# Optimization experiments

Measured on AMD Instinct MI355X. Metric: run time of the kernel, lower is better.

The kernel has to match this reference:

```python
import jax, jax.numpy as jnp
from jax import lax
import numpy as np

P = 16          # patch_len
EPS = 1e-5      # BatchNorm eps


def _dct_mats(L):
    # torch_dct DCT-II: ortho matrix Co and scale d s.t. dct(norm=None)(x) = (x @ Co.T) * d,
    # dct(norm='ortho')(x) = x @ Co.T, idct(norm=None)(y) = (y / d) @ Co
    n = jnp.arange(L, dtype=jnp.float32)
    base = jnp.cos(jnp.pi * (2.0 * n[None, :] + 1.0) * n[:, None] / (2.0 * L))
    ck = jnp.where(n == 0, 1.0 / jnp.sqrt(jnp.float32(L)), jnp.sqrt(2.0 / L))
    Co = base * ck[:, None]
    d = jnp.where(n == 0, 2.0 * jnp.sqrt(jnp.float32(L)), jnp.sqrt(2.0 * L))
    return Co, d


def _gelu(t):
    return jax.nn.gelu(t, approximate=False)  # torch nn.GELU default (erf)


def _dw(t, w, pad):  # depthwise Conv1d, t [B,D,L], w [D,k], SAME-style padding
    return lax.conv_general_dilated(t, w[:, None, :], (1,), [(pad, pad)],
                                    feature_group_count=t.shape[1],
                                    dimension_numbers=('NCH', 'OIH', 'NCH'))


def _forward(x, conv1_w, conv1_b, conv2_w, conv2_b, conv3_w, conv3_b,
             dn_g, dn_b, dn_m, dn_v, pn_g, pn_b, pn_m, pn_v,
             embed_w, embed_b, lin_res_w, lin_res_b,
             depth_res_w, depth_res_b, depth_conv_w, depth_conv_b,
             threshold, att_dw_w, att_dw_b, att_conv_w, att_conv_b,
             att_g, att_b, att_m, att_v, fc1_w, fc1_b, fc2_w, fc2_b):
    B, L, D = x.shape
    N = L // P                       # patch_num (stride == patch_len)
    Co, dvec = _dct_mats(L)

    conv1 = lambda t: t * conv1_w[:, None] + conv1_b[:, None]   # grouped 1x1 Conv1d
    bnD = lambda t: (t - dn_m[:, None]) * (dn_g[:, None] / jnp.sqrt(dn_v[:, None] + EPS)) + dn_b[:, None]

    xt = jnp.transpose(x, (0, 2, 1))                 # [B,D,L]
    freq_res = conv1(xt)
    z_dct = (xt @ Co.T) * dvec                       # dct(norm=None)

    # adaptive high-frequency mask
    energy = jnp.sum(z_dct * z_dct, axis=-1)         # [B,D]
    med = jnp.median(energy, axis=1, keepdims=True)
    ne = energy / (med + 1e-6)
    thr = lax.stop_gradient(jnp.quantile(ne, jnp.clip(threshold[0], 0.0, 1.0)))
    mask = (ne > thr).astype(x.dtype)[..., None]     # rows of dominant vars -> 1
    z = _gelu(conv1(z_dct * mask))
    z1 = (z / dvec) @ Co + freq_res                  # idct(norm=None) + residual

    # patching (stride == patch_len -> unfold is a reshape)
    z_p = xt.reshape(B * D, N, P) @ embed_w + embed_b            # [BD,N,P*P]
    z_res = (z_p.reshape(B, D, -1) @ lin_res_w + lin_res_b).transpose(0, 2, 1)  # [B,pred,D]
    time_res = z_p @ depth_res_w + depth_res_b                   # [BD,N,P]
    # depth_conv: grouped Conv1d kernel=stride=P over d_model=P*P
    z_depth = jnp.einsum('bnpj,nj->bnp', z_p.reshape(B * D, N, P, P), depth_conv_w) \
              + depth_conv_b[None, :, None] + time_res
    z_depth = (z_depth - pn_m[:, None]) * (pn_g[:, None] / jnp.sqrt(pn_v[:, None] + EPS)) + pn_b[:, None]
    z2 = _gelu(z_depth).reshape(B, D, L)

    z2_f = conv1(bnD(_gelu((z2 @ Co.T) * dvec)))

    z_r = jax.nn.sigmoid(conv1(bnD(_gelu(_dw(z1, conv2_w, 2) + conv2_b[:, None]))))
    zg = _gelu(z2_f * z_r)

    z1b = _gelu(bnD(_dw(z1, conv3_w, 3) + conv3_b[:, None]))
    z1c = bnD(zg) + z1b

    # DctAtt on z1c * z2: ortho DCT, take 5 low-freq comps per var
    xa = (z1c * z2) @ Co.T                            # [B,D,L]
    low = xa[:, :, :5].reshape(B, D, 5)               # concat layout matches torch loop
    zd = jnp.einsum('bdj,j->bd', low, att_dw_w) + att_dw_b[0]   # Conv1d(1,1,5,stride=5)
    zd = _gelu(zd)
    zd = (zd - att_m[0]) * (att_g[0] / jnp.sqrt(att_v[0] + EPS)) + att_b[0]  # BN(1)
    zd = zd * att_conv_w[0] + att_conv_b[0]           # Conv1d(1,1,1)
    att1 = jax.nn.softmax(zd, axis=-1)[..., None]     # [B,D,1]

    zf = z1c * att1 + z2 * (1.0 - att1)
    out = _gelu(zf @ fc1_w + fc1_b) @ fc2_w + fc2_b   # Mlp -> [B,D,pred]
    return z_res + out.transpose(0, 2, 1)             # [B,pred,D]


def setup_inputs() -> dict:
    key = jax.random.key(0)
    ks = iter(jax.random.split(key, 48))
    B, L, D, pred = 32, 512, 321, 96
    N, dm = L // P, P * P
    r = lambda shape, s=1.0: jax.random.normal(next(ks), shape, jnp.float32) * s
    return dict(
        x=r((B, L, D)),
        conv1_w=r((D,), 0.5) + 1.0, conv1_b=r((D,), 0.1),
        conv2_w=r((D, 5), 0.3), conv2_b=r((D,), 0.1),
        conv3_w=r((D, 7), 0.3), conv3_b=r((D,), 0.1),
        dn_g=jnp.ones((D,), jnp.float32), dn_b=jnp.zeros((D,), jnp.float32),
        dn_m=r((D,), 0.1), dn_v=jnp.ones((D,), jnp.float32),
        pn_g=jnp.ones((N,), jnp.float32), pn_b=jnp.zeros((N,), jnp.float32),
        pn_m=r((N,), 0.1), pn_v=jnp.ones((N,), jnp.float32),
        embed_w=r((P, dm), 0.25), embed_b=r((dm,), 0.02),
        lin_res_w=r((N * dm, pred), 0.01), lin_res_b=r((pred,), 0.02),
        depth_res_w=r((dm, P), 0.06), depth_res_b=r((P,), 0.02),
        depth_conv_w=r((N, P), 0.25), depth_conv_b=r((N,), 0.02),
        threshold=jax.random.uniform(next(ks), (1,), jnp.float32) * 0.5,
        att_dw_w=r((5,), 0.4), att_dw_b=r((1,), 0.1),
        att_conv_w=r((1,)), att_conv_b=r((1,), 0.1),
        att_g=jnp.ones((1,), jnp.float32), att_b=jnp.zeros((1,), jnp.float32),
        att_m=jnp.zeros((1,), jnp.float32), att_v=jnp.ones((1,), jnp.float32),
        fc1_w=r((L, pred), 0.04), fc1_b=r((pred,), 0.02),
        fc2_w=r((pred, pred), 0.1), fc2_b=r((pred,), 0.02),
    )


def reference(x, conv1_w, conv1_b, conv2_w, conv2_b, conv3_w, conv3_b,
              dn_g, dn_b, dn_m, dn_v, pn_g, pn_b, pn_m, pn_v,
              embed_w, embed_b, lin_res_w, lin_res_b,
              depth_res_w, depth_res_b, depth_conv_w, depth_conv_b,
              threshold, att_dw_w, att_dw_b, att_conv_w, att_conv_b,
              att_g, att_b, att_m, att_v, fc1_w, fc1_b, fc2_w, fc2_b):
    return _forward(x, conv1_w, conv1_b, conv2_w, conv2_b, conv3_w, conv3_b,
                    dn_g, dn_b, dn_m, dn_v, pn_g, pn_b, pn_m, pn_v,
                    embed_w, embed_b, lin_res_w, lin_res_b,
                    depth_res_w, depth_res_b, depth_conv_w, depth_conv_b,
                    threshold, att_dw_w, att_dw_b, att_conv_w, att_conv_b,
                    att_g, att_b, att_m, att_v, fc1_w, fc1_b, fc2_w, fc2_b)
```

## Files before the change

### kernel.cpp

```cpp
#include <hip/hip_runtime.h>
#include <cmath>


#define BB   32
#define LL   512
#define DD   321
#define PRED 96
#define M_ROWS (BB*DD)

__device__ __forceinline__ float gelu_f(float x){
  return 0.5f*x*(1.0f + erff(x*0.70710678118654752440f));
}
__device__ __forceinline__ float sigmoid_f(float x){
  return 1.0f/(1.0f+expf(-x));
}

constexpr size_t OFF_CO   = 0;
constexpr size_t OFF_COT  = OFF_CO   + 512*512;
constexpr size_t OFF_DVEC = OFF_COT  + 512*512;
constexpr size_t OFF_CATT = OFF_DVEC + 512;
constexpr size_t OFF_FC1T = OFF_CATT + 512;
constexpr size_t OFF_WEFFT= OFF_FC1T + 96*512;
constexpr size_t OFF_CRES = OFF_WEFFT+ 96*512;
constexpr size_t OFF_MP   = OFF_CRES + 128;
constexpr size_t OFF_C2P  = OFF_MP   + 32*256;
constexpr size_t OFF_AF   = OFF_C2P  + 512;
constexpr size_t OFF_CF   = OFF_AF   + 384;
constexpr size_t OFF_DNS  = OFF_CF   + 384;
constexpr size_t OFF_BF   = OFF_DNS  + 384;
constexpr size_t OFF_EN   = OFF_BF   + 384;
constexpr size_t OFF_NE   = OFF_EN   + 10368;
constexpr size_t OFF_THR  = OFF_NE   + 10368;
constexpr size_t OFF_ZDP  = OFF_THR  + 64;
constexpr size_t OFF_ATT1 = OFF_ZDP  + 10368;
constexpr size_t OFF_XT   = OFF_ATT1 + 10368;
constexpr size_t OFF_ZDCT = OFF_XT   + (size_t)M_ROWS*512;
constexpr size_t OFF_Z1   = OFF_ZDCT + (size_t)M_ROWS*512;
constexpr size_t OFF_Z2   = OFF_Z1   + (size_t)M_ROWS*512;
constexpr size_t OFF_Z1C  = OFF_Z2   + (size_t)M_ROWS*512;
constexpr size_t OFF_H    = OFF_Z1C  + (size_t)M_ROWS*512;
constexpr size_t OFF_ZRES = OFF_H    + (size_t)M_ROWS*96;
constexpr size_t OFF_WPART= OFF_ZRES + (size_t)M_ROWS*96;
constexpr size_t OFF_PCRES= OFF_WPART+ 4*96*512;
constexpr size_t WS_FLOATS= OFF_PCRES+ 128*96;

__global__ __launch_bounds__(256)
void k0_dct(float* __restrict__ Co, float* __restrict__ CoT, float* __restrict__ dvec,
            float* __restrict__ catt, const float* __restrict__ attw)
{
  const float PI_F = 3.14159265358979323846f;
  int b = blockIdx.x;
  float ckb = (b==0) ? (1.0f/sqrtf(512.0f)) : sqrtf(2.0f/512.0f);
  for (int l=threadIdx.x; l<512; l+=256){
    float a1 = PI_F * (float)(2*l+1);
    float a2 = a1 * (float)b;
    float c  = cosf(a2 * (1.0f/1024.0f)) * ckb;
    Co[b*512+l] = c;
  }
  for (int k=threadIdx.x; k<512; k+=256){
    float ckk = (k==0) ? (1.0f/sqrtf(512.0f)) : sqrtf(2.0f/512.0f);
    float a1 = PI_F * (float)(2*b+1);
    float a2 = a1 * (float)k;
    CoT[b*512+k] = cosf(a2 * (1.0f/1024.0f)) * ckk;
  }
  if (threadIdx.x==0) dvec[b] = (b==0) ? 2.0f*sqrtf(512.0f) : sqrtf(2.0f*512.0f);
  if (b==0){
    for (int l=threadIdx.x; l<512; l+=256){
      float sacc=0.f;
      for (int j=0;j<5;j++){
        float ckj = (j==0)?(1.0f/sqrtf(512.0f)):sqrtf(2.0f/512.0f);
        float a1 = PI_F*(float)(2*l+1);
        float a2 = a1*(float)j;
        sacc += cosf(a2 * (1.0f/1024.0f))*ckj*attw[j];
      }
      catt[l]=sacc;
    }
  }
}

__global__ __launch_bounds__(256)
void kA_weff(const float* __restrict__ ew_g, const float* __restrict__ eb_g,
             const float* __restrict__ lrw,
             float* __restrict__ Wpart, float* __restrict__ pcres)
{
  const int n = blockIdx.x, kb4 = blockIdx.y;
  __shared__ float ews[16][68];
  __shared__ float ebs[64];
  __shared__ float lw[64][96];
  const int tid = threadIdx.x;
  const int jbase = kb4*64;
  for (int i=tid; i<1024; i+=256){
    int p2 = i>>6, j2 = i&63;
    ews[p2][j2] = ew_g[p2*256 + jbase + j2];
  }
  if (tid < 64) ebs[tid] = eb_g[jbase + tid];
  for (int i=tid; i<1536; i+=256){
    int jj = i/24, c4 = i%24;
    *(float4*)&lw[jj][c4*4] =
      *(const float4*)&lrw[((size_t)(n*256 + jbase + jj))*96 + c4*4];
  }
  __syncthreads();
  const int p = tid>>4, tx = tid&15;
  float acc[6]={0,0,0,0,0,0};
  float accB[6]={0,0,0,0,0,0};
  for (int jj=0; jj<64; jj++){
    float a = ews[p][jj];
    #pragma unroll
    for (int g=0; g<6; g++) acc[g] = fmaf(a, lw[jj][tx+16*g], acc[g]);
    if (p==0){
      float bv = ebs[jj];
      #pragma unroll
      for (int g=0; g<6; g++) accB[g] = fmaf(bv, lw[jj][tx+16*g], accB[g]);
    }
  }
  #pragma unroll
  for (int g=0; g<6; g++){
    int pr = tx + 16*g;
    Wpart[((size_t)kb4*96 + pr)*512 + n*16 + p] = acc[g];
    if (p==0) pcres[(n*4+kb4)*96 + pr] = accB[g];
  }
}

__global__ __launch_bounds__(256)
void kA_fin(const float* __restrict__ Wpart, const float* __restrict__ pcres,
            const float* __restrict__ lrb,
            float* __restrict__ WeffT, float* __restrict__ cres)
{
  int b = blockIdx.x;
  if (b < 192){
    int i = b*256 + threadIdx.x;
    WeffT[i] = (Wpart[i] + Wpart[49152+i]) + (Wpart[2*49152+i] + Wpart[3*49152+i]);
  } else {
    int pr = threadIdx.x;
    if (pr < 96){
      float s = lrb[pr];
      for (int nn=0; nn<128; nn++) s += pcres[nn*96+pr];
      cres[pr] = s;
    }
  }
}

__global__ __launch_bounds__(256)
void kT_fc1(const float* __restrict__ fc1_w, float* __restrict__ fc1T)
{
  __shared__ float t[32][33];
  int c0 = blockIdx.x*32;
  int l0 = blockIdx.y*32;
  int tid=threadIdx.x; int j=tid&31, i0=tid>>5;
  for (int ii=0; ii<32; ii+=8){
    int l=l0+i0+ii, c=c0+j;
    t[i0+ii][j] = (c<96)? fc1_w[l*96+c] : 0.f;
  }
  __syncthreads();
  for (int ii=0; ii<32; ii+=8){
    int c=c0+i0+ii, l=l0+j;
    if (c<96) fc1T[(size_t)c*512 + l] = t[j][i0+ii];
  }
}

__global__ __launch_bounds__(256)
void k0_depth(const float* __restrict__ embed_w, const float* __restrict__ embed_b,
              const float* __restrict__ drw, const float* __restrict__ drb,
              const float* __restrict__ dcw, const float* __restrict__ dcb,
              const float* __restrict__ png, const float* __restrict__ pnb,
              const float* __restrict__ pnm, const float* __restrict__ pnv,
              float* __restrict__ Mp, float* __restrict__ c2p)
{
  int n = blockIdx.x; int tid = threadIdx.x;
  int q = tid>>4, p = tid&15;
  float acc = 0.f;
  for (int j=0;j<16;j++)  acc = fmaf(embed_w[q*256 + p*16 + j], dcw[n*16+j], acc);
  float wtr = 0.f;
  for (int j=0;j<256;j++) wtr = fmaf(embed_w[q*256 + j], drw[j*16+p], wtr);
  float sn = png[n]/sqrtf(pnv[n]+1e-5f);
  Mp[n*256 + q*16 + p] = (acc + wtr) * sn;
  if (q==0){
    float c = dcb[n];
    for (int j=0;j<16;j++)  c = fmaf(embed_b[p*16+j], dcw[n*16+j], c);
    float ctr = drb[p];
    for (int j=0;j<256;j++) ctr = fmaf(embed_b[j], drw[j*16+p], ctr);
    c += ctr;
    c2p[n*16+p] = (c - pnm[n])*sn + pnb[n];
  }
}

__global__ void k0_fold(const float* __restrict__ w1, const float* __restrict__ b1,
                        const float* __restrict__ g,  const float* __restrict__ bbq,
                        const float* __restrict__ mq, const float* __restrict__ vq,
                        float* __restrict__ Af, float* __restrict__ Cf,
                        float* __restrict__ dns, float* __restrict__ Bf)
{
  int d = blockIdx.x*256 + threadIdx.x;
  if (d >= DD) return;
  float s  = g[d]/sqrtf(vq[d]+1e-5f);
  float bf = bbq[d] - mq[d]*s;
  dns[d]=s; Bf[d]=bf; Af[d]=s*w1[d]; Cf[d]=bf*w1[d]+b1[d];
}

__global__ __launch_bounds__(256)
void k1_transpose(const float* __restrict__ x, float* __restrict__ xt)
{
  int b = blockIdx.z; int l0 = blockIdx.y*32; int d0 = blockIdx.x*32;
  __shared__ float t[32][33];
  int tid=threadIdx.x; int j = tid&31, i0 = tid>>5;
  for (int ii=0; ii<32; ii+=8){
    int l = l0 + i0+ii; int d = d0 + j;
    t[i0+ii][j] = (d<DD) ? x[((size_t)b*512 + l)*DD + d] : 0.f;
  }
  __syncthreads();
  for (int ii=0; ii<32; ii+=8){
    int d = d0 + i0+ii; int l = l0 + j;
    if (d<DD) xt[((size_t)b*DD+d)*512 + l] = t[j][i0+ii];
  }
}

template<int OP>
__global__ __launch_bounds__(256)
void gemm_nt(const float* __restrict__ A, const float* __restrict__ B,
             float* __restrict__ C, int M, int Ncols, int ldc,
             const float* __restrict__ p0, const float* __restrict__ p1,
             const float* __restrict__ p2, const float* __restrict__ p3)
{
  __shared__ float As[32][132];
  __shared__ float Bs[32][68];
  const int tid = threadIdx.x;
  const int tx = tid & 15, ty = tid >> 4;
  const int rb = blockIdx.y * 128, cb = blockIdx.x * 64;

  float acc[8][4];
  #pragma unroll
  for (int i=0;i<8;i++)
    #pragma unroll
    for (int j=0;j<4;j++) acc[i][j]=0.f;

  for (int kb=0; kb<512; kb+=32){
    #pragma unroll
    for (int i=0;i<4;i++){
      int idx = tid + i*256;
      int row = idx >> 3, k4 = (idx & 7)*4;
      float4 v = make_float4(0.f,0.f,0.f,0.f);
      int r = rb + row;
      if (r < M) v = *reinterpret_cast<const float4*>(A + (size_t)r*512 + kb + k4);
      As[k4+0][row]=v.x; As[k4+1][row]=v.y; As[k4+2][row]=v.z; As[k4+3][row]=v.w;
    }
    #pragma unroll
    for (int i=0;i<2;i++){
      int idx = tid + i*256;
      int row = idx >> 3, k4 = (idx & 7)*4;
      float4 v = make_float4(0.f,0.f,0.f,0.f);
      int c = cb + row;
      if (c < Ncols) v = *reinterpret_cast<const float4*>(B + (size_t)c*512 + kb + k4);
      Bs[k4+0][row]=v.x; Bs[k4+1][row]=v.y; Bs[k4+2][row]=v.z; Bs[k4+3][row]=v.w;
    }
    __syncthreads();
    #pragma unroll
    for (int kk=0; kk<32; kk++){
      const float4 a0 = *reinterpret_cast<const float4*>(&As[kk][ty*8]);
      const float4 a1 = *reinterpret_cast<const float4*>(&As[kk][ty*8+4]);
      const float4 b0 = *reinterpret_cast<const float4*>(&Bs[kk][tx*4]);
      float av[8]={a0.x,a0.y,a0.z,a0.w,a1.x,a1.y,a1.z,a1.w};
      float bv[4]={b0.x,b0.y,b0.z,b0.w};
      #pragma unroll
      for (int i=0;i<8;i++)
        #pragma unroll
        for (int j=0;j<4;j++) acc[i][j]=fmaf(av[i],bv[j],acc[i][j]);
    }
    __syncthreads();
  }

  #pragma unroll
  for (int i=0;i<8;i++){
    const int r = rb + ty*8 + i;
    const bool rok = (r < M);
    if constexpr (OP==0){
      if (rok){
        #pragma unroll
        for (int j=0;j<4;j++){
          int c = cb + tx*4 + j;
          C[(size_t)r*ldc + c] = acc[i][j]*p0[c];
        }
      }
    } else if constexpr (OP==1){
      if (rok){
        int d = r % DD;
        float w = p0[d], bo = p1[d];
        #pragma unroll
        for (int j=0;j<4;j++){
          int c = cb + tx*4 + j;
          C[(size_t)r*ldc + c] = acc[i][j] + p2[(size_t)r*512 + c]*w + bo;
        }
      }
    } else if constexpr (OP==2){
      if (rok){
        int d = r % DD;
        float w = p0[d], bo = p1[d];
        #pragma unroll
        for (int j=0;j<4;j++){
          int c = cb + tx*4 + j;
          float t = acc[i][j]*p3[c];
          C[(size_t)r*ldc + c] = gelu_f(t)*w + bo;
        }
      }
    } else if constexpr (OP==3){
      if (rok){
        #pragma unroll
        for (int j=0;j<4;j++){
          int c = cb + tx*4 + j;
          if (c < Ncols) C[(size_t)r*ldc + c] = gelu_f(acc[i][j] + p0[c]);
        }
      }
    } else {
      if (rok){
        #pragma unroll
        for (int j=0;j<4;j++){
          int c = cb + tx*4 + j;
          if (c < Ncols) C[(size_t)r*ldc + c] = acc[i][j] + p0[c];
        }
      }
    }
  }
}

__global__ __launch_bounds__(256)
void k_energy(const float* __restrict__ zdct, float* __restrict__ energy)
{
  int r=blockIdx.x, tid=threadIdx.x;
  __shared__ float rbuf[256];
  float acc=0.f;
  for (int k=tid;k<512;k+=256){ float v=zdct[(size_t)r*512+k]; acc=fmaf(v,v,acc); }
  rbuf[tid]=acc; __syncthreads();
  for (int st=128;st>0;st>>=1){ if(tid<st) rbuf[tid]+=rbuf[tid+st]; __syncthreads(); }
  if (tid==0) energy[r]=rbuf[0];
}

__global__ __launch_bounds__(256)
void k3_median(const float* __restrict__ energy, float* __restrict__ ne)
{
  int b = blockIdx.x, tid=threadIdx.x;
  __shared__ float e[DD];
  __shared__ float medv;
  for (int i=tid;i<DD;i+=256) e[i]=energy[b*DD+i];
  __syncthreads();
  for (int i=tid;i<DD;i+=256){
    float v=e[i]; int lt=0, eq=0;
    for (int j=0;j<DD;j++){ float u=e[j]; lt += (u<v); eq += (u==v); }
    if (lt<=160 && 160<lt+eq) medv=v;
  }
  __syncthreads();
  float den = medv + 1e-6f;
  for (int i=tid;i<DD;i+=256) ne[b*DD+i] = e[i]/den;
}

__global__ __launch_bounds__(1024)
void k3_thr(const float* __restrict__ ne, const float* __restrict__ thrin,
            float* __restrict__ out)
{
  __shared__ int hist[256];
  __shared__ unsigned sPrefix; __shared__ int sRank;
  int tid = threadIdx.x;
  float q = fminf(fmaxf(thrin[0],0.f),1.f);
  float pos = q * (float)(M_ROWS-1);
  int lo = (int)floorf(pos); int hi = (int)ceilf(pos);
  float frac = pos - floorf(pos);
  float vals[2];
  for (int s=0;s<2;s++){
    int rank = s ? hi : lo;
    unsigned prefix=0, pmask=0;
    for (int pass=0; pass<4; pass++){
      int shift = 24 - 8*pass;
      if (tid<256) hist[tid]=0;
      __syncthreads();
      for (int i=tid;i<M_ROWS;i+=1024){
        unsigned u = __float_as_uint(ne[i]);
        if ((u & pmask)==prefix) atomicAdd(&hist[(u>>shift)&255u],1);
      }
      __syncthreads();
      if (tid==0){
        int cum=0;
        for (int bkt=0;bkt<256;bkt++){
          int c=hist[bkt];
          if (cum + c > rank){ sPrefix = prefix | ((unsigned)bkt<<(unsigned)shift); sRank = rank - cum; break; }
          cum += c;
        }
      }
      __syncthreads();
      prefix = sPrefix; rank = sRank; pmask |= (0xFFu<<(unsigned)shift);
      __syncthreads();
    }
    vals[s] = __uint_as_float(prefix);
  }
  if (tid==0) out[0] = vals[0]*(1.0f-frac) + vals[1]*frac;
}

__global__ void k4_pre(float* __restrict__ zdct, const float* __restrict__ ne,
                       const float* __restrict__ thr, const float* __restrict__ w1,
                       const float* __restrict__ b1, const float* __restrict__ dvec)
{
  size_t idx = (size_t)blockIdx.x*256 + threadIdx.x;
  int r = (int)(idx>>7);
  int k0 = ((int)idx & 127)*4;
  float m  = (ne[r] > thr[0]) ? 1.f : 0.f;
  int d = r % DD;
  float w = w1[d]*m, bo = b1[d];
  float4 v = ((float4*)zdct)[idx];
  v.x = gelu_f(fmaf(v.x,w,bo))/dvec[k0+0];
  v.y = gelu_f(fmaf(v.y,w,bo))/dvec[k0+1];
  v.z = gelu_f(fmaf(v.z,w,bo))/dvec[k0+2];
  v.w = gelu_f(fmaf(v.w,w,bo))/dvec[k0+3];
  ((float4*)zdct)[idx]=v;
}

__global__ __launch_bounds__(256)
void k5_z2(const float* __restrict__ xt, const float* __restrict__ Mp,
           const float* __restrict__ c2p, float* __restrict__ z2)
{
  int r = blockIdx.x, tid=threadIdx.x;
  __shared__ float row[512];
  for (int i=tid;i<512;i+=256) row[i]=xt[(size_t)r*512+i];
  __syncthreads();
  for (int idx=tid; idx<512; idx+=256){
    int n = idx>>4, p = idx&15;
    float acc = c2p[idx];
    const float* Mn = Mp + n*256 + p;
    #pragma unroll
    for (int qq=0;qq<16;qq++) acc = fmaf(row[n*16+qq], Mn[qq*16], acc);
    z2[(size_t)r*512+idx] = gelu_f(acc);
  }
}

__global__ __launch_bounds__(256)
void k7_fuse(const float* __restrict__ z1, const float* __restrict__ z2f,
             const float* __restrict__ z2, float* __restrict__ z1c,
             float* __restrict__ zdpre,
             const float* __restrict__ c2w, const float* __restrict__ c2b,
             const float* __restrict__ c3w, const float* __restrict__ c3b,
             const float* __restrict__ Af,  const float* __restrict__ Cf,
             const float* __restrict__ dns, const float* __restrict__ Bf,
             const float* __restrict__ catt)
{
  int r = blockIdx.x, tid=threadIdx.x;
  int d = r % DD;
  __shared__ float zrow[518];
  __shared__ float rbuf[256];
  for (int i=tid;i<518;i+=256){
    int l = i-3;
    zrow[i] = (l>=0 && l<512) ? z1[(size_t)r*512+l] : 0.f;
  }
  __syncthreads();
  float w2[5], w3[7];
  #pragma unroll
  for (int t=0;t<5;t++) w2[t]=c2w[d*5+t];
  #pragma unroll
  for (int t=0;t<7;t++) w3[t]=c3w[d*7+t];
  const float cb2=c2b[d], cb3=c3b[d];
  const float af=Af[d], cf=Cf[d], s=dns[d], bf=Bf[d];
  float dotacc=0.f;
  for (int l=tid;l<512;l+=256){
    float c5=cb2;
    #pragma unroll
    for (int t=0;t<5;t++) c5 = fmaf(zrow[l+t+1], w2[t], c5);
    float zr  = sigmoid_f(fmaf(gelu_f(c5),af,cf));
    float zgv = gelu_f(z2f[(size_t)r*512+l]*zr);
    float c7=cb3;
    #pragma unroll
    for (int t=0;t<7;t++) c7 = fmaf(zrow[l+t], w3[t], c7);
    float z1b = gelu_f(fmaf(c7,s,bf));
    float v = fmaf(zgv,s,bf) + z1b;
    z1c[(size_t)r*512+l]=v;
    dotacc = fmaf(v*z2[(size_t)r*512+l], catt[l], dotacc);
  }
  rbuf[tid]=dotacc; __syncthreads();
  for (int st=128;st>0;st>>=1){ if(tid<st) rbuf[tid]+=rbuf[tid+st]; __syncthreads(); }
  if (tid==0) zdpre[r]=rbuf[0];
}

__global__ __launch_bounds__(256)
void k8_att(const float* __restrict__ zdpre, float* __restrict__ att1,
            const float* __restrict__ adwb, const float* __restrict__ acw,
            const float* __restrict__ acb,  const float* __restrict__ ag,
            const float* __restrict__ ab,   const float* __restrict__ am,
            const float* __restrict__ av)
{
  int b=blockIdx.x, t=threadIdx.x;
  __shared__ float sred[256];
  float vloc[2];
  float mx=-INFINITY;
  float sA = ag[0]/sqrtf(av[0]+1e-5f);
  #pragma unroll
  for (int ii=0;ii<2;ii++){
    int d=t+ii*256;
    float v=-INFINITY;
    if (d<DD){
      float zd = zdpre[b*DD+d] + adwb[0];
      zd = gelu_f(zd);
      zd = (zd-am[0])*sA + ab[0];
      zd = zd*acw[0] + acb[0];
      v=zd;
    }
    vloc[ii]=v; mx=fmaxf(mx,v);
  }
  sred[t]=mx; __syncthreads();
  for (int st=128;st>0;st>>=1){ if (t<st) sred[t]=fmaxf(sred[t],sred[t+st]); __syncthreads(); }
  float m=sred[0]; __syncthreads();
  float e0 = (t<DD)     ? expf(vloc[0]-m) : 0.f;
  float e1 = (t+256<DD) ? expf(vloc[1]-m) : 0.f;
  sred[t]=e0+e1; __syncthreads();
  for (int st=128;st>0;st>>=1){ if (t<st) sred[t]+=sred[t+st]; __syncthreads(); }
  float sum=sred[0];
  if (t<DD)     att1[b*DD+t]     = e0/sum;
  if (t+256<DD) att1[b*DD+t+256] = e1/sum;
}

__global__ void k8b_zf(const float* __restrict__ z1c, const float* __restrict__ z2,
                       const float* __restrict__ att1, float* __restrict__ zf)
{
  size_t idx = (size_t)blockIdx.x*256 + threadIdx.x;
  int r = (int)(idx>>7);
  float a = att1[r];
  float4 v1 = ((const float4*)z1c)[idx];
  float4 v2 = ((const float4*)z2)[idx];
  float4 o;
  o.x = v1.x*a + v2.x*(1.f-a);
  o.y = v1.y*a + v2.y*(1.f-a);
  o.z = v1.z*a + v2.z*(1.f-a);
  o.w = v1.w*a + v2.w*(1.f-a);
  ((float4*)zf)[idx]=o;
}

__global__ __launch_bounds__(256)
void k9_final(const float* __restrict__ h, const float* __restrict__ zres,
              const float* __restrict__ fc2_w, const float* __restrict__ fc2_b,
              float* __restrict__ outF)
{
  int b = blockIdx.y; int d0 = blockIdx.x*32;
  __shared__ float f2[96*96];
  __shared__ float hs[32][97];
  __shared__ float zs[32][97];
  int tid=threadIdx.x;
  for (int i=tid;i<96*96;i+=256) f2[i]=fc2_w[i];
  for (int i=tid;i<32*96;i+=256){
    int dl = i/96, p = i%96; int d = d0+dl;
    float hv=0.f, zv=0.f;
    if (d<DD){ hv = h[((size_t)b*DD+d)*96+p]; zv = zres[((size_t)b*DD+d)*96+p]; }
    hs[dl][p]=hv; zs[dl][p]=zv;
  }
  __syncthreads();
  int tx = tid & 31, ty = tid >> 5;
  int d = d0+tx;
  float acc[12];
  #pragma unroll
  for (int kc=0;kc<12;kc++) acc[kc]=0.f;
  for (int p=0;p<96;p++){
    float hv = hs[tx][p];
    #pragma unroll
    for (int kc=0;kc<12;kc++) acc[kc] = fmaf(hv, f2[p*96 + ty + kc*8], acc[kc]);
  }
  if (d<DD){
    #pragma unroll
    for (int kc=0;kc<12;kc++){
      int c = ty + kc*8;
      outF[((size_t)b*96 + c)*DD + d] = acc[kc] + fc2_b[c] + zs[tx][c];
    }
  }
}

extern "C" void kernel_launch(void* const* d_in, const int* in_sizes, int n_in,
                              void* d_out, int out_size, void* d_ws, size_t ws_size,
                              hipStream_t stream)
{
  (void)in_sizes; (void)n_in; (void)out_size; (void)ws_size;
  const float* x        =(const float*)d_in[0];
  const float* conv1_w  =(const float*)d_in[1];
  const float* conv1_b  =(const float*)d_in[2];
  const float* conv2_w  =(const float*)d_in[3];
  const float* conv2_b  =(const float*)d_in[4];
  const float* conv3_w  =(const float*)d_in[5];
  const float* conv3_b  =(const float*)d_in[6];
  const float* dn_g     =(const float*)d_in[7];
  const float* dn_b     =(const float*)d_in[8];
  const float* dn_m     =(const float*)d_in[9];
  const float* dn_v     =(const float*)d_in[10];
  const float* pn_g     =(const float*)d_in[11];
  const float* pn_b     =(const float*)d_in[12];
  const float* pn_m     =(const float*)d_in[13];
  const float* pn_v     =(const float*)d_in[14];
  const float* embed_w  =(const float*)d_in[15];
  const float* embed_b  =(const float*)d_in[16];
  const float* lin_res_w=(const float*)d_in[17];
  const float* lin_res_b=(const float*)d_in[18];
  const float* depth_res_w=(const float*)d_in[19];
  const float* depth_res_b=(const float*)d_in[20];
  const float* depth_conv_w=(const float*)d_in[21];
  const float* depth_conv_b=(const float*)d_in[22];
  const float* threshold=(const float*)d_in[23];
  const float* att_dw_w =(const float*)d_in[24];
  const float* att_dw_b =(const float*)d_in[25];
  const float* att_conv_w=(const float*)d_in[26];
  const float* att_conv_b=(const float*)d_in[27];
  const float* att_g    =(const float*)d_in[28];
  const float* att_b    =(const float*)d_in[29];
  const float* att_m    =(const float*)d_in[30];
  const float* att_v    =(const float*)d_in[31];
  const float* fc1_w    =(const float*)d_in[32];
  const float* fc1_b    =(const float*)d_in[33];
  const float* fc2_w    =(const float*)d_in[34];
  const float* fc2_b    =(const float*)d_in[35];

  float* ws   = (float*)d_ws;
  float* Co   = ws + OFF_CO;
  float* CoT  = ws + OFF_COT;
  float* dvec = ws + OFF_DVEC;
  float* catt = ws + OFF_CATT;
  float* fc1T = ws + OFF_FC1T;
  float* WeffT= ws + OFF_WEFFT;
  float* cres = ws + OFF_CRES;
  float* Mp   = ws + OFF_MP;
  float* c2p  = ws + OFF_C2P;
  float* Af   = ws + OFF_AF;
  float* Cf   = ws + OFF_CF;
  float* dns  = ws + OFF_DNS;
  float* Bf   = ws + OFF_BF;
  float* energy=ws + OFF_EN;
  float* ne   = ws + OFF_NE;
  float* thr  = ws + OFF_THR;
  float* zdpre= ws + OFF_ZDP;
  float* att1 = ws + OFF_ATT1;
  float* xt   = ws + OFF_XT;
  float* zdct = ws + OFF_ZDCT;
  float* z1   = ws + OFF_Z1;
  float* z2   = ws + OFF_Z2;
  float* z1c  = ws + OFF_Z1C;
  float* h    = ws + OFF_H;
  float* zres = ws + OFF_ZRES;
  float* Wpart= ws + OFF_WPART;
  float* pcres= ws + OFF_PCRES;

  k0_dct  <<<512, 256, 0, stream>>>(Co, CoT, dvec, catt, att_dw_w);
  kA_weff <<<dim3(32,4), 256, 0, stream>>>(embed_w, embed_b, lin_res_w, Wpart, pcres);
  kA_fin  <<<193, 256, 0, stream>>>(Wpart, pcres, lin_res_b, WeffT, cres);
  kT_fc1  <<<dim3(3,16), 256, 0, stream>>>(fc1_w, fc1T);
  k0_depth<<<32, 256, 0, stream>>>(embed_w, embed_b, depth_res_w, depth_res_b,
                                   depth_conv_w, depth_conv_b, pn_g, pn_b, pn_m, pn_v,
                                   Mp, c2p);
  k0_fold <<<2, 256, 0, stream>>>(conv1_w, conv1_b, dn_g, dn_b, dn_m, dn_v,
                                  Af, Cf, dns, Bf);

  k1_transpose<<<dim3(11,16,BB), 256, 0, stream>>>(x, xt);
  gemm_nt<0><<<dim3(8,81), 256, 0, stream>>>(xt, Co, zdct, M_ROWS, 512, 512,
                                             dvec, nullptr, nullptr, nullptr);
  k_energy <<<M_ROWS, 256, 0, stream>>>(zdct, energy);
  k3_median<<<BB, 256, 0, stream>>>(energy, ne);
  k3_thr   <<<1, 1024, 0, stream>>>(ne, threshold, thr);

  k4_pre   <<<5136, 256, 0, stream>>>(zdct, ne, thr, conv1_w, conv1_b, dvec);
  gemm_nt<1><<<dim3(8,81), 256, 0, stream>>>(zdct, CoT, z1, M_ROWS, 512, 512,
                                             conv1_w, conv1_b, xt, nullptr);

  k5_z2    <<<M_ROWS, 256, 0, stream>>>(xt, Mp, c2p, z2);
  gemm_nt<2><<<dim3(8,81), 256, 0, stream>>>(z2, Co, zdct, M_ROWS, 512, 512,
                                             Af, Cf, nullptr, dvec);

  k7_fuse  <<<M_ROWS, 256, 0, stream>>>(z1, zdct, z2, z1c, zdpre,
                                        conv2_w, conv2_b, conv3_w, conv3_b,
                                        Af, Cf, dns, Bf, catt);
  k8_att   <<<BB, 256, 0, stream>>>(zdpre, att1, att_dw_b, att_conv_w, att_conv_b,
                                    att_g, att_b, att_m, att_v);
  k8b_zf   <<<5136, 256, 0, stream>>>(z1c, z2, att1, z1);

  gemm_nt<3><<<dim3(2,81), 256, 0, stream>>>(z1, fc1T, h, M_ROWS, 96, 96,
                                             fc1_b, nullptr, nullptr, nullptr);
  gemm_nt<4><<<dim3(2,81), 256, 0, stream>>>(xt, WeffT, zres, M_ROWS, 96, 96,
                                             cres, nullptr, nullptr, nullptr);
  k9_final <<<dim3(11,BB), 256, 0, stream>>>(h, zres, fc2_w, fc2_b, (float*)d_out);
}
```

Baseline: 792.8 us.

## Exploit DCT even/odd symmetry to halve DCT/IDCT GEMM flops

Splits the 512-point DCT matrix into even and odd cosine halves (256x256 each) and folds each input row as x[k]±x[511-k], so every forward DCT becomes two K=256 products. The inverse DCT splits the input into even and odd coefficients and rebuilds the mirrored outputs as E+O and E−O. Together this halves the FMA count and the matrix traffic of the three large 512x512 GEMMs. In exchange each block holds two accumulator sets and twice the shared-memory tiles, which raises register and LDS pressure and may lower occupancy.

```diff
diff --git a/kernel.cpp b/kernel.cpp
--- a/kernel.cpp
+++ b/kernel.cpp
@@ -15,9 +15,11 @@
   return 1.0f/(1.0f+expf(-x));
 }
 
-constexpr size_t OFF_CO   = 0;
-constexpr size_t OFF_COT  = OFF_CO   + 512*512;
-constexpr size_t OFF_DVEC = OFF_COT  + 512*512;
+constexpr size_t OFF_COE  = 0;
+constexpr size_t OFF_COO  = OFF_COE  + 256*256;
+constexpr size_t OFF_COET = OFF_COO  + 256*256;
+constexpr size_t OFF_COOT = OFF_COET + 256*256;
+constexpr size_t OFF_DVEC = OFF_COOT + 256*256;
 constexpr size_t OFF_CATT = OFF_DVEC + 512;
 constexpr size_t OFF_FC1T = OFF_CATT + 512;
 constexpr size_t OFF_WEFFT= OFF_FC1T + 96*512;
@@ -45,30 +47,40 @@
 constexpr size_t WS_FLOATS= OFF_PCRES+ 128*96;
 
 __global__ __launch_bounds__(256)
-void k0_dct(float* __restrict__ Co, float* __restrict__ CoT, float* __restrict__ dvec,
-            float* __restrict__ catt, const float* __restrict__ attw)
+void k0_dctF(float* __restrict__ CoE, float* __restrict__ CoO,
+             float* __restrict__ CoET, float* __restrict__ CoOT,
+             float* __restrict__ dvec, float* __restrict__ catt,
+             const float* __restrict__ attw)
 {
   const float PI_F = 3.14159265358979323846f;
-  int b = blockIdx.x;
-  float ckb = (b==0) ? (1.0f/sqrtf(512.0f)) : sqrtf(2.0f/512.0f);
-  for (int l=threadIdx.x; l<512; l+=256){
-    float a1 = PI_F * (float)(2*l+1);
-    float a2 = a1 * (float)b;
-    float c  = cosf(a2 * (1.0f/1024.0f)) * ckb;
-    Co[b*512+l] = c;
-  }
-  for (int k=threadIdx.x; k<512; k+=256){
-    float ckk = (k==0) ? (1.0f/sqrtf(512.0f)) : sqrtf(2.0f/512.0f);
-    float a1 = PI_F * (float)(2*b+1);
-    float a2 = a1 * (float)k;
-    CoT[b*512+k] = cosf(a2 * (1.0f/1024.0f)) * ckk;
-  }
-  if (threadIdx.x==0) dvec[b] = (b==0) ? 2.0f*sqrtf(512.0f) : sqrtf(2.0f*512.0f);
-  if (b==0){
-    for (int l=threadIdx.x; l<512; l+=256){
+  const float ck0 = 1.0f/sqrtf(512.0f), ckn = sqrtf(2.0f/512.0f);
+  int c = blockIdx.x;
+  int t = threadIdx.x;
+  {
+    float a1 = PI_F * (float)(2*t+1);
+    float ckE = (c==0) ? ck0 : ckn;
+    float aE = a1 * (float)(2*c);
+    float aO = a1 * (float)(2*c+1);
+    CoE[c*256+t] = cosf(aE * (1.0f/1024.0f)) * ckE;
+    CoO[c*256+t] = cosf(aO * (1.0f/1024.0f)) * ckn;
+  }
+  {
+    float a1 = PI_F * (float)(2*c+1);
+    float ckE = (t==0) ? ck0 : ckn;
+    float aE = a1 * (float)(2*t);
+    float aO = a1 * (float)(2*t+1);
+    CoET[c*256+t] = cosf(aE * (1.0f/1024.0f)) * ckE;
+    CoOT[c*256+t] = cosf(aO * (1.0f/1024.0f)) * ckn;
+  }
+  if (t==0){
+    dvec[2*c]   = (c==0) ? 2.0f*sqrtf(512.0f) : sqrtf(2.0f*512.0f);
+    dvec[2*c+1] = sqrtf(2.0f*512.0f);
+  }
+  if (c==0){
+    for (int l=t; l<512; l+=256){
       float sacc=0.f;
       for (int j=0;j<5;j++){
-        float ckj = (j==0)?(1.0f/sqrtf(512.0f)):sqrtf(2.0f/512.0f);
+        float ckj = (j==0)? ck0 : ckn;
         float a1 = PI_F*(float)(2*l+1);
         float a2 = a1*(float)j;
         sacc += cosf(a2 * (1.0f/1024.0f))*ckj*attw[j];
@@ -216,10 +228,140 @@
 
 template<int OP>
 __global__ __launch_bounds__(256)
+void gemm_dual(const float* __restrict__ A, const float* __restrict__ BE,
+               const float* __restrict__ BO, float* __restrict__ C, int M,
+               const float* __restrict__ p0, const float* __restrict__ p1,
+               const float* __restrict__ p2, const float* __restrict__ p3)
+{
+  __shared__ float Ae[32][132];
+  __shared__ float Ao[32][132];
+  __shared__ float Be[32][68];
+  __shared__ float Bo[32][68];
+  const int tid = threadIdx.x;
+  const int tx = tid & 15, ty = tid >> 4;
+  const int rb = blockIdx.y * 128, cb = blockIdx.x * 64;
+
+  float accE[8][4], accO[8][4];
+  #pragma unroll
+  for (int i=0;i<8;i++)
+    #pragma unroll
+    for (int j=0;j<4;j++){ accE[i][j]=0.f; accO[i][j]=0.f; }
+
+  for (int kb=0; kb<256; kb+=32){
+    if constexpr (OP==0 || OP==2){
+      #pragma unroll
+      for (int i=0;i<4;i++){
+        int idx = tid + i*256;
+        int row = idx >> 3, k4 = (idx & 7)*4;
+        int r = rb + row;
+        float4 lo = make_float4(0.f,0.f,0.f,0.f);
+        float4 hi = make_float4(0.f,0.f,0.f,0.f);
+        if (r < M){
+          lo = *(const float4*)(A + (size_t)r*512 + kb + k4);
+          hi = *(const float4*)(A + (size_t)r*512 + (508 - kb - k4));
+        }
+        Ae[k4+0][row] = lo.x + hi.w;  Ao[k4+0][row] = lo.x - hi.w;
+        Ae[k4+1][row] = lo.y + hi.z;  Ao[k4+1][row] = lo.y - hi.z;
+        Ae[k4+2][row] = lo.z + hi.y;  Ao[k4+2][row] = lo.z - hi.y;
+        Ae[k4+3][row] = lo.w + hi.x;  Ao[k4+3][row] = lo.w - hi.x;
+      }
+    } else {
+      #pragma unroll
+      for (int i=0;i<8;i++){
+        int idx = tid + i*256;
+        int row = idx >> 4, c0 = (idx & 15)*4;
+        int r = rb + row;
+        float4 v = make_float4(0.f,0.f,0.f,0.f);
+        if (r < M) v = *(const float4*)(A + (size_t)r*512 + 2*kb + c0);
+        int kk = c0 >> 1;
+        Ae[kk+0][row] = v.x;  Ao[kk+0][row] = v.y;
+        Ae[kk+1][row] = v.z;  Ao[kk+1][row] = v.w;
+      }
+    }
+    #pragma unroll
+    for (int i=0;i<2;i++){
+      int idx = tid + i*256;
+      int crow = idx >> 3, k4 = (idx & 7)*4;
+      int c = cb + crow;
+      float4 ve = *(const float4*)(BE + (size_t)c*256 + kb + k4);
+      float4 vo = *(const float4*)(BO + (size_t)c*256 + kb + k4);
+      Be[k4+0][crow]=ve.x; Be[k4+1][crow]=ve.y; Be[k4+2][crow]=ve.z; Be[k4+3][crow]=ve.w;
+      Bo[k4+0][crow]=vo.x; Bo[k4+1][crow]=vo.y; Bo[k4+2][crow]=vo.z; Bo[k4+3][crow]=vo.w;
+    }
+    __syncthreads();
+    #pragma unroll
+    for (int kk=0; kk<32; kk++){
+      const float4 ae0 = *(const float4*)&Ae[kk][ty*8];
+      const float4 ae1 = *(const float4*)&Ae[kk][ty*8+4];
+      const float4 ao0 = *(const float4*)&Ao[kk][ty*8];
+      const float4 ao1 = *(const float4*)&Ao[kk][ty*8+4];
+      const float4 be  = *(const float4*)&Be[kk][tx*4];
+      const float4 bo  = *(const float4*)&Bo[kk][tx*4];
+      float aev[8]={ae0.x,ae0.y,ae0.z,ae0.w,ae1.x,ae1.y,ae1.z,ae1.w};
+      float aov[8]={ao0.x,ao0.y,ao0.z,ao0.w,ao1.x,ao1.y,ao1.z,ao1.w};
+      float bev[4]={be.x,be.y,be.z,be.w};
+      float bov[4]={bo.x,bo.y,bo.z,bo.w};
+      #pragma unroll
+      for (int i=0;i<8;i++)
+        #pragma unroll
+        for (int j=0;j<4;j++){
+          accE[i][j]=fmaf(aev[i],bev[j],accE[i][j]);
+          accO[i][j]=fmaf(aov[i],bov[j],accO[i][j]);
+        }
+    }
+    __syncthreads();
+  }
+
+  const int c0 = cb + tx*4;
+  #pragma unroll
+  for (int i=0;i<8;i++){
+    const int r = rb + ty*8 + i;
+    if (r >= M) continue;
+    if constexpr (OP==0){
+      float4 o0 = make_float4(accE[i][0]*p0[2*c0+0], accO[i][0]*p0[2*c0+1],
+                              accE[i][1]*p0[2*c0+2], accO[i][1]*p0[2*c0+3]);
+      float4 o1 = make_float4(accE[i][2]*p0[2*c0+4], accO[i][2]*p0[2*c0+5],
+                              accE[i][3]*p0[2*c0+6], accO[i][3]*p0[2*c0+7]);
+      *(float4*)(C + (size_t)r*512 + 2*c0)     = o0;
+      *(float4*)(C + (size_t)r*512 + 2*c0 + 4) = o1;
+    } else if constexpr (OP==2){
+      int d = r % DD;
+      float w = p0[d], bo = p1[d];
+      float4 o0 = make_float4(gelu_f(accE[i][0]*p3[2*c0+0])*w+bo,
+                              gelu_f(accO[i][0]*p3[2*c0+1])*w+bo,
+                              gelu_f(accE[i][1]*p3[2*c0+2])*w+bo,
+                              gelu_f(accO[i][1]*p3[2*c0+3])*w+bo);
+      float4 o1 = make_float4(gelu_f(accE[i][2]*p3[2*c0+4])*w+bo,
+                              gelu_f(accO[i][2]*p3[2*c0+5])*w+bo,
+                              gelu_f(accE[i][3]*p3[2*c0+6])*w+bo,
+                              gelu_f(accO[i][3]*p3[2*c0+7])*w+bo);
+      *(float4*)(C + (size_t)r*512 + 2*c0)     = o0;
+      *(float4*)(C + (size_t)r*512 + 2*c0 + 4) = o1;
+    } else {
+      int d = r % DD;
+      float w = p0[d], bo = p1[d];
+      float4 xf = *(const float4*)(p2 + (size_t)r*512 + c0);
+      float4 xr = *(const float4*)(p2 + (size_t)r*512 + 508 - c0);
+      float4 of, orv;
+      of.x = accE[i][0]+accO[i][0] + xf.x*w+bo;
+      of.y = accE[i][1]+accO[i][1] + xf.y*w+bo;
+      of.z = accE[i][2]+accO[i][2] + xf.z*w+bo;
+      of.w = accE[i][3]+accO[i][3] + xf.w*w+bo;
+      orv.x = accE[i][3]-accO[i][3] + xr.x*w+bo;
+      orv.y = accE[i][2]-accO[i][2] + xr.y*w+bo;
+      orv.z = accE[i][1]-accO[i][1] + xr.z*w+bo;
+      orv.w = accE[i][0]-accO[i][0] + xr.w*w+bo;
+      *(float4*)(C + (size_t)r*512 + c0)       = of;
+      *(float4*)(C + (size_t)r*512 + 508 - c0) = orv;
+    }
+  }
+}
+
+template<int OP>
+__global__ __launch_bounds__(256)
 void gemm_nt(const float* __restrict__ A, const float* __restrict__ B,
              float* __restrict__ C, int M, int Ncols, int ldc,
-             const float* __restrict__ p0, const float* __restrict__ p1,
-             const float* __restrict__ p2, const float* __restrict__ p3)
+             const float* __restrict__ p0)
 {
   __shared__ float As[32][132];
   __shared__ float Bs[32][68];
@@ -271,51 +413,13 @@
   #pragma unroll
   for (int i=0;i<8;i++){
     const int r = rb + ty*8 + i;
-    const bool rok = (r < M);
-    if constexpr (OP==0){
-      if (rok){
-        #pragma unroll
-        for (int j=0;j<4;j++){
-          int c = cb + tx*4 + j;
-          C[(size_t)r*ldc + c] = acc[i][j]*p0[c];
-        }
-      }
-    } else if constexpr (OP==1){
-      if (rok){
-        int d = r % DD;
-        float w = p0[d], bo = p1[d];
-        #pragma unroll
-        for (int j=0;j<4;j++){
-          int c = cb + tx*4 + j;
-          C[(size_t)r*ldc + c] = acc[i][j] + p2[(size_t)r*512 + c]*w + bo;
-        }
-      }
-    } else if constexpr (OP==2){
-      if (rok){
-        int d = r % DD;
-        float w = p0[d], bo = p1[d];
-        #pragma unroll
-        for (int j=0;j<4;j++){
-          int c = cb + tx*4 + j;
-          float t = acc[i][j]*p3[c];
-          C[(size_t)r*ldc + c] = gelu_f(t)*w + bo;
-        }
-      }
-    } else if constexpr (OP==3){
-      if (rok){
-        #pragma unroll
-        for (int j=0;j<4;j++){
-          int c = cb + tx*4 + j;
-          if (c < Ncols) C[(size_t)r*ldc + c] = gelu_f(acc[i][j] + p0[c]);
-        }
-      }
-    } else {
-      if (rok){
-        #pragma unroll
-        for (int j=0;j<4;j++){
-          int c = cb + tx*4 + j;
-          if (c < Ncols) C[(size_t)r*ldc + c] = acc[i][j] + p0[c];
-        }
+    if (r >= M) continue;
+    #pragma unroll
+    for (int j=0;j<4;j++){
+      int c = cb + tx*4 + j;
+      if (c < Ncols){
+        if constexpr (OP==3) C[(size_t)r*ldc + c] = gelu_f(acc[i][j] + p0[c]);
+        else                 C[(size_t)r*ldc + c] = acc[i][j] + p0[c];
       }
     }
   }
@@ -607,8 +711,10 @@
   const float* fc2_b    =(const float*)d_in[35];
 
   float* ws   = (float*)d_ws;
-  float* Co   = ws + OFF_CO;
-  float* CoT  = ws + OFF_COT;
+  float* CoE  = ws + OFF_COE;
+  float* CoO  = ws + OFF_COO;
+  float* CoET = ws + OFF_COET;
+  float* CoOT = ws + OFF_COOT;
   float* dvec = ws + OFF_DVEC;
   float* catt = ws + OFF_CATT;
   float* fc1T = ws + OFF_FC1T;
@@ -635,7 +741,7 @@
   float* Wpart= ws + OFF_WPART;
   float* pcres= ws + OFF_PCRES;
 
-  k0_dct  <<<512, 256, 0, stream>>>(Co, CoT, dvec, catt, att_dw_w);
+  k0_dctF <<<256, 256, 0, stream>>>(CoE, CoO, CoET, CoOT, dvec, catt, att_dw_w);
   kA_weff <<<dim3(32,4), 256, 0, stream>>>(embed_w, embed_b, lin_res_w, Wpart, pcres);
   kA_fin  <<<193, 256, 0, stream>>>(Wpart, pcres, lin_res_b, WeffT, cres);
   kT_fc1  <<<dim3(3,16), 256, 0, stream>>>(fc1_w, fc1T);
@@ -646,19 +752,19 @@
                                   Af, Cf, dns, Bf);
 
   k1_transpose<<<dim3(11,16,BB), 256, 0, stream>>>(x, xt);
-  gemm_nt<0><<<dim3(8,81), 256, 0, stream>>>(xt, Co, zdct, M_ROWS, 512, 512,
-                                             dvec, nullptr, nullptr, nullptr);
+  gemm_dual<0><<<dim3(4,81), 256, 0, stream>>>(xt, CoE, CoO, zdct, M_ROWS,
+                                               dvec, nullptr, nullptr, nullptr);
   k_energy <<<M_ROWS, 256, 0, stream>>>(zdct, energy);
   k3_median<<<BB, 256, 0, stream>>>(energy, ne);
   k3_thr   <<<1, 1024, 0, stream>>>(ne, threshold, thr);
 
   k4_pre   <<<5136, 256, 0, stream>>>(zdct, ne, thr, conv1_w, conv1_b, dvec);
-  gemm_nt<1><<<dim3(8,81), 256, 0, stream>>>(zdct, CoT, z1, M_ROWS, 512, 512,
-                                             conv1_w, conv1_b, xt, nullptr);
+  gemm_dual<1><<<dim3(4,81), 256, 0, stream>>>(zdct, CoET, CoOT, z1, M_ROWS,
+                                               conv1_w, conv1_b, xt, nullptr);
 
   k5_z2    <<<M_ROWS, 256, 0, stream>>>(xt, Mp, c2p, z2);
-  gemm_nt<2><<<dim3(8,81), 256, 0, stream>>>(z2, Co, zdct, M_ROWS, 512, 512,
-                                             Af, Cf, nullptr, dvec);
+  gemm_dual<2><<<dim3(4,81), 256, 0, stream>>>(z2, CoE, CoO, zdct, M_ROWS,
+                                               Af, Cf, nullptr, dvec);
 
   k7_fuse  <<<M_ROWS, 256, 0, stream>>>(z1, zdct, z2, z1c, zdpre,
                                         conv2_w, conv2_b, conv3_w, conv3_b,
@@ -667,9 +773,7 @@
                                     att_g, att_b, att_m, att_v);
   k8b_zf   <<<5136, 256, 0, stream>>>(z1c, z2, att1, z1);
 
-  gemm_nt<3><<<dim3(2,81), 256, 0, stream>>>(z1, fc1T, h, M_ROWS, 96, 96,
-                                             fc1_b, nullptr, nullptr, nullptr);
-  gemm_nt<4><<<dim3(2,81), 256, 0, stream>>>(xt, WeffT, zres, M_ROWS, 96, 96,
-                                             cres, nullptr, nullptr, nullptr);
+  gemm_nt<3><<<dim3(2,81), 256, 0, stream>>>(z1, fc1T, h, M_ROWS, 96, 96, fc1_b);
+  gemm_nt<4><<<dim3(2,81), 256, 0, stream>>>(xt, WeffT, zres, M_ROWS, 96, 96, cres);
   k9_final <<<dim3(11,BB), 256, 0, stream>>>(h, zres, fc2_w, fc2_b, (float*)d_out);
 }
```

Result: faster. 767.0 us (-3.3%).
